# Optimization experiments

Hardware: AMD Instinct MI355X
Metric: run time of the kernel (lower is better)

The kernel has to match this reference:

```python
import jax, jax.numpy as jnp
import numpy as np

HEAD_DIM = 64

def setup_inputs() -> dict:
    key = jax.random.key(0)
    k1, k2, k3 = jax.random.split(key, 3)
    B, L, D = 2, 2048, 1024
    x = jax.random.normal(k1, (B, L, D), dtype=jnp.float32)
    # torch nn.Linear weights are [out_features, in_features]
    w_qkv = jax.random.normal(k2, (3 * D, D), dtype=jnp.float32) * (D ** -0.5)
    w_out = jax.random.normal(k3, (D, D), dtype=jnp.float32) * (D ** -0.5)
    # causal mask: True = attend (masked_fill on logical_not)
    mask = jnp.tril(jnp.ones((L, L), dtype=bool))[None].repeat(B, axis=0)
    return {"x": x, "mask": mask, "w_qkv": w_qkv, "w_out": w_out}

def reference(x, mask, w_qkv, w_out):
    B, L, D = x.shape
    H, Hd = D // HEAD_DIM, HEAD_DIM
    scale = Hd ** -0.5
    qkv = x @ w_qkv.T                               # [B, L, 3D]
    q, k, v = jnp.split(qkv, 3, axis=-1)
    # [B, L, D] -> [B, H, L, Hd]
    def split_heads(t):
        return t.reshape(B, L, H, Hd).transpose(0, 2, 1, 3)
    q, k, v = split_heads(q), split_heads(k), split_heads(v)
    attn = jnp.einsum('bhld,bhmd->bhlm', q, k) * scale  # [B, H, L, L]
    attn = jnp.where(mask[:, None, :, :], attn, -jnp.inf)
    attn = jax.nn.softmax(attn, axis=-1)
    out = jnp.einsum('bhlm,bhmd->bhld', attn, v)        # [B, H, L, Hd]
    out = out.transpose(0, 2, 1, 3).reshape(B, L, D)
    return out @ w_out.T
```

## Files before the change

### kernel.cpp

```cpp
#include <hip/hip_runtime.h>
#include <hip/hip_bf16.h>


typedef __bf16 bf16;
typedef __bf16 bf16x8 __attribute__((ext_vector_type(8)));
typedef __bf16 bf16x4 __attribute__((ext_vector_type(4)));
typedef float  f32x4  __attribute__((ext_vector_type(4)));

#define MFMA16(a, b, c) __builtin_amdgcn_mfma_f32_16x16x32_bf16(a, b, c, 0, 0, 0)

__global__ __launch_bounds__(256) void cvt_all(
    const float* __restrict__ x, const float* __restrict__ wq,
    const float* __restrict__ wo, bf16* __restrict__ dst) {
  int i = blockIdx.x * 256 + threadIdx.x;
  const float* src;
  int off;
  if (i < 1048576) {
    src = x; off = i;
  } else if (i < 1048576 + 786432) {
    src = wq; off = i - 1048576;
  } else {
    src = wo; off = i - (1048576 + 786432);
  }
  float4 v = ((const float4*)src)[off];
  bf16x4 o;
  o[0] = (bf16)v.x; o[1] = (bf16)v.y; o[2] = (bf16)v.z; o[3] = (bf16)v.w;
  ((bf16x4*)dst)[i] = o;
}

__device__ __forceinline__ void gload_lds16(const bf16* g, bf16* l) {
  __builtin_amdgcn_global_load_lds(
      (const __attribute__((address_space(1))) void*)g,
      (__attribute__((address_space(3))) void*)l, 16, 0, 0);
}

template <int ROWS>
__device__ __forceinline__ void stage_tile(const bf16* __restrict__ src, int ld,
                                           bf16* lds, int tid) {
  const int wid = tid >> 6;
#pragma unroll
  for (int i = 0; i < ROWS / 32; ++i) {
    int c = i * 256 + tid;
    int row = c >> 3;
    int slot = (c & 7) ^ (row & 7);
    gload_lds16(src + row * ld + slot * 8, lds + i * 2048 + wid * 512);
  }
}

__device__ __forceinline__ bf16x8 read_swz(const bf16* lds, int row, int kbyte) {
  int byte = row * 128 + (kbyte ^ ((row & 7) << 4));
  return *(const bf16x8*)((const char*)lds + byte);
}

template <int MODE>
__global__ __launch_bounds__(256) void gemm_nt(
    const bf16* __restrict__ A, const bf16* __restrict__ Bt,
    bf16* __restrict__ C0, bf16* __restrict__ C1, bf16* __restrict__ C2,
    float* __restrict__ Cf,
    int M, int N, int K, int nbm) {
  __shared__ bf16 ldsA[128 * 64];
  __shared__ bf16 ldsB[128 * 64];
  const int tid = threadIdx.x;
  const int lane = tid & 63, wid = tid >> 6;
  const int wr = wid >> 1, wc = wid & 1;
  const int bm = blockIdx.x % nbm, bn = blockIdx.x / nbm;
  const int l15 = lane & 15, g = lane >> 4;

  f32x4 acc[4][4] = {};
  const bf16* Ab = A + (size_t)bm * 128 * K;
  const bf16* Bb = Bt + (size_t)bn * 128 * K;

  for (int k0 = 0; k0 < K; k0 += 64) {
    __syncthreads();
    stage_tile<128>(Ab + k0, K, ldsA, tid);
    stage_tile<128>(Bb + k0, K, ldsB, tid);
    __syncthreads();
#pragma unroll
    for (int kc = 0; kc < 2; ++kc) {
      bf16x8 af[4], bfr[4];
#pragma unroll
      for (int mi = 0; mi < 4; ++mi)
        af[mi] = read_swz(ldsA, wr * 64 + mi * 16 + l15, kc * 64 + g * 16);
#pragma unroll
      for (int ni = 0; ni < 4; ++ni)
        bfr[ni] = read_swz(ldsB, wc * 64 + ni * 16 + l15, kc * 64 + g * 16);
#pragma unroll
      for (int mi = 0; mi < 4; ++mi)
#pragma unroll
        for (int ni = 0; ni < 4; ++ni)
          acc[mi][ni] = MFMA16(af[mi], bfr[ni], acc[mi][ni]);
    }
  }

  const int mbase = bm * 128 + wr * 64, nbase = bn * 128 + wc * 64;
#pragma unroll
  for (int mi = 0; mi < 4; ++mi) {
#pragma unroll
    for (int ni = 0; ni < 4; ++ni) {
#pragma unroll
      for (int r = 0; r < 4; ++r) {
        int m = mbase + mi * 16 + g * 4 + r;
        int n = nbase + ni * 16 + l15;
        if (MODE == 0) {
          Cf[(size_t)m * N + n] = acc[mi][ni][r];
        } else {
          bf16 v = (bf16)acc[mi][ni][r];
          int part = n >> 10;
          int hh = (n >> 6) & 15, hd = n & 63;
          int bb = m >> 11, ll = m & 2047;
          size_t bhb = (size_t)(bb * 16 + hh);
          if (part == 2) {
            C2[(bhb * 64 + hd) * 2048 + ll] = v;
          } else {
            bf16* dst = (part == 0) ? C0 : C1;
            dst[(bhb * 2048 + ll) * 64 + hd] = v;
          }
        }
      }
    }
  }
}

__global__ __launch_bounds__(256) void attn_fwd(
    const bf16* __restrict__ Q, const bf16* __restrict__ Kb,
    const bf16* __restrict__ Vt, bf16* __restrict__ O2) {
  __shared__ bf16 ldsK[2][64 * 64];
  __shared__ bf16 ldsVt[2][64 * 64];
  __shared__ bf16 ldsP[4][16 * 72];

  const int tid = threadIdx.x, lane = tid & 63, wid = tid >> 6;
  const int l15 = lane & 15, g = lane >> 4;
  const int qt = 31 - (blockIdx.x >> 5);
  const int bh = blockIdx.x & 31;
  const int b = bh >> 4, h = bh & 15;
  const bf16* Qh  = Q  + (size_t)bh * 2048 * 64;
  const bf16* Kh  = Kb + (size_t)bh * 2048 * 64;
  const bf16* VtH = Vt + (size_t)bh * 64 * 2048;
  const int q0 = qt * 64;
  const int qrow = q0 + wid * 16 + l15;

  bf16x8 qf[2];
#pragma unroll
  for (int dk = 0; dk < 2; ++dk)
    qf[dk] = *(const bf16x8*)(Qh + (size_t)qrow * 64 + dk * 32 + g * 8);

  float m_run = -__builtin_inff(), l_run = 0.f;
  f32x4 oacc[4] = {};

  auto step = [&](bool masked, int curb) {
    f32x4 s[4] = {};
#pragma unroll
    for (int sub = 0; sub < 4; ++sub) {
#pragma unroll
      for (int dk = 0; dk < 2; ++dk) {
        bf16x8 kf = read_swz(&ldsK[curb][0], sub * 16 + l15, dk * 64 + g * 16);
        s[sub] = MFMA16(kf, qf[dk], s[sub]);
      }
    }
    float pvv[16];
    float mtile = -__builtin_inff();
#pragma unroll
    for (int sub = 0; sub < 4; ++sub)
#pragma unroll
      for (int r = 0; r < 4; ++r) {
        float v = s[sub][r] * 0.125f;
        if (masked) {
          int kvl = sub * 16 + g * 4 + r;
          if (kvl > wid * 16 + l15) v = -__builtin_inff();
        }
        pvv[sub * 4 + r] = v;
        mtile = fmaxf(mtile, v);
      }
    mtile = fmaxf(mtile, __shfl_xor(mtile, 16));
    mtile = fmaxf(mtile, __shfl_xor(mtile, 32));
    float mnew = fmaxf(m_run, mtile);
    float alpha = __expf(m_run - mnew);
    float lsum = 0.f;
#pragma unroll
    for (int sub = 0; sub < 4; ++sub) {
      bf16x4 pb;
#pragma unroll
      for (int r = 0; r < 4; ++r) {
        float e = __expf(pvv[sub * 4 + r] - mnew);
        lsum += e;
        pb[r] = (bf16)e;
      }
      *(bf16x4*)(&ldsP[wid][l15 * 72 + sub * 16 + g * 4]) = pb;
    }
    lsum += __shfl_xor(lsum, 16);
    lsum += __shfl_xor(lsum, 32);
    l_run = alpha * l_run + lsum;
    m_run = mnew;
#pragma unroll
    for (int dsub = 0; dsub < 4; ++dsub) {
      oacc[dsub][0] *= alpha; oacc[dsub][1] *= alpha;
      oacc[dsub][2] *= alpha; oacc[dsub][3] *= alpha;
    }
#pragma unroll
    for (int kc = 0; kc < 2; ++kc) {
      bf16x8 pf = *(const bf16x8*)(&ldsP[wid][l15 * 72 + kc * 32 + g * 8]);
#pragma unroll
      for (int dsub = 0; dsub < 4; ++dsub) {
        bf16x8 vf = read_swz(&ldsVt[curb][0], dsub * 16 + l15, kc * 64 + g * 16);
        oacc[dsub] = MFMA16(vf, pf, oacc[dsub]);
      }
    }
  };

  stage_tile<64>(Kh, 64, &ldsK[0][0], tid);
  stage_tile<64>(VtH, 2048, &ldsVt[0][0], tid);
  __syncthreads();

  int cur = 0;
  for (int t = 0; t < qt; ++t) {
    stage_tile<64>(Kh + (size_t)(t + 1) * 64 * 64, 64, &ldsK[cur ^ 1][0], tid);
    stage_tile<64>(VtH + (t + 1) * 64, 2048, &ldsVt[cur ^ 1][0], tid);
    step(false, cur);
    __syncthreads();
    cur ^= 1;
  }
  step(true, cur);

  const float linv = 1.f / l_run;
#pragma unroll
  for (int dsub = 0; dsub < 4; ++dsub)
#pragma unroll
    for (int r = 0; r < 4; ++r) {
      int d = dsub * 16 + g * 4 + r;
      O2[((size_t)(b * 2048 + qrow)) * 1024 + h * 64 + d] =
          (bf16)(oacc[dsub][r] * linv);
    }
}

extern "C" void kernel_launch(void* const* d_in, const int* in_sizes, int n_in,
                              void* d_out, int out_size, void* d_ws, size_t ws_size,
                              hipStream_t stream) {
  const float* x     = (const float*)d_in[0];
  const float* w_qkv = (const float*)d_in[2];
  const float* w_out = (const float*)d_in[3];
  float* out = (float*)d_out;

  char* ws = (char*)d_ws;
  bf16* xb    = (bf16*)(ws);
  bf16* wqkvb = (bf16*)(ws + ((size_t)8 << 20));
  bf16* woutb = (bf16*)(ws + ((size_t)14 << 20));
  bf16* Qb    = (bf16*)(ws + ((size_t)16 << 20));
  bf16* Kbuf  = (bf16*)(ws + ((size_t)24 << 20));
  bf16* Vtb   = (bf16*)(ws + ((size_t)32 << 20));
  bf16* O2    = (bf16*)(ws + ((size_t)40 << 20));

  cvt_all<<<dim3(8192), 256, 0, stream>>>(x, w_qkv, w_out, xb);

  gemm_nt<1><<<dim3(32 * 24), 256, 0, stream>>>(xb, wqkvb, Qb, Kbuf, Vtb,
                                                nullptr, 4096, 3072, 1024, 32);
  attn_fwd<<<dim3(32 * 32), 256, 0, stream>>>(Qb, Kbuf, Vtb, O2);
  gemm_nt<0><<<dim3(32 * 8), 256, 0, stream>>>(O2, woutb, nullptr, nullptr,
                                               nullptr, out, 4096, 1024, 1024, 32);
}
```

Baseline: 205.7 us.

## Streamline attention softmax: exp2 with folded scale, lazy rescale, deferred row-sum reduction

Reworks the online softmax in the attention kernel. The 1/sqrt(d) scale and log2(e) are folded into one constant so exponentials use exp2f on raw scores. The accumulator rescale is skipped when no lane's running max grows, and the row-sum cross-lane reduction moves out of the loop to the end. The P staging buffer switches from padded rows to the same XOR swizzle used for K/V tiles. Together these cut per-tile ALU and shuffle work, at the cost of a wave-wide vote branch and a changed LDS addressing pattern.

Measured after the change: 199.1 us. 3.2% less time.

```diff
diff --git a/kernel.cpp b/kernel.cpp
--- a/kernel.cpp
+++ b/kernel.cpp
@@ -126,7 +126,7 @@
     const bf16* __restrict__ Vt, bf16* __restrict__ O2) {
   __shared__ bf16 ldsK[2][64 * 64];
   __shared__ bf16 ldsVt[2][64 * 64];
-  __shared__ bf16 ldsP[4][16 * 72];
+  __shared__ bf16 ldsP[4][16 * 64];
 
   const int tid = threadIdx.x, lane = tid & 63, wid = tid >> 6;
   const int l15 = lane & 15, g = lane >> 4;
@@ -139,12 +139,15 @@
   const int q0 = qt * 64;
   const int qrow = q0 + wid * 16 + l15;
 
+  const float CE = 0.18033688011112042f;
+
   bf16x8 qf[2];
 #pragma unroll
   for (int dk = 0; dk < 2; ++dk)
     qf[dk] = *(const bf16x8*)(Qh + (size_t)qrow * 64 + dk * 32 + g * 8);
 
-  float m_run = -__builtin_inff(), l_run = 0.f;
+  float m_run = -__builtin_inff();
+  float l_lane = 0.f;
   f32x4 oacc[4] = {};
 
   auto step = [&](bool masked, int curb) {
@@ -157,48 +160,51 @@
         s[sub] = MFMA16(kf, qf[dk], s[sub]);
       }
     }
-    float pvv[16];
-    float mtile = -__builtin_inff();
-#pragma unroll
-    for (int sub = 0; sub < 4; ++sub)
-#pragma unroll
-      for (int r = 0; r < 4; ++r) {
-        float v = s[sub][r] * 0.125f;
-        if (masked) {
+    if (masked) {
+#pragma unroll
+      for (int sub = 0; sub < 4; ++sub)
+#pragma unroll
+        for (int r = 0; r < 4; ++r) {
           int kvl = sub * 16 + g * 4 + r;
-          if (kvl > wid * 16 + l15) v = -__builtin_inff();
+          if (kvl > wid * 16 + l15) s[sub][r] = -__builtin_inff();
         }
-        pvv[sub * 4 + r] = v;
-        mtile = fmaxf(mtile, v);
-      }
-    mtile = fmaxf(mtile, __shfl_xor(mtile, 16));
-    mtile = fmaxf(mtile, __shfl_xor(mtile, 32));
-    float mnew = fmaxf(m_run, mtile);
-    float alpha = __expf(m_run - mnew);
+    }
+    float m0 = fmaxf(fmaxf(s[0][0], s[0][1]), fmaxf(s[0][2], s[0][3]));
+    float m1 = fmaxf(fmaxf(s[1][0], s[1][1]), fmaxf(s[1][2], s[1][3]));
+    float m2 = fmaxf(fmaxf(s[2][0], s[2][1]), fmaxf(s[2][2], s[2][3]));
+    float m3 = fmaxf(fmaxf(s[3][0], s[3][1]), fmaxf(s[3][2], s[3][3]));
+    float mt = fmaxf(fmaxf(m0, m1), fmaxf(m2, m3));
+    mt = fmaxf(mt, __shfl_xor(mt, 16));
+    mt = fmaxf(mt, __shfl_xor(mt, 32));
+    if (!__all(mt <= m_run)) {
+      float mnew = fmaxf(m_run, mt);
+      float alpha = exp2f((m_run - mnew) * CE);
+#pragma unroll
+      for (int dsub = 0; dsub < 4; ++dsub) {
+        oacc[dsub][0] *= alpha; oacc[dsub][1] *= alpha;
+        oacc[dsub][2] *= alpha; oacc[dsub][3] *= alpha;
+      }
+      l_lane *= alpha;
+      m_run = mnew;
+    }
     float lsum = 0.f;
 #pragma unroll
     for (int sub = 0; sub < 4; ++sub) {
       bf16x4 pb;
 #pragma unroll
       for (int r = 0; r < 4; ++r) {
-        float e = __expf(pvv[sub * 4 + r] - mnew);
+        float e = exp2f((s[sub][r] - m_run) * CE);
         lsum += e;
         pb[r] = (bf16)e;
       }
-      *(bf16x4*)(&ldsP[wid][l15 * 72 + sub * 16 + g * 4]) = pb;
-    }
-    lsum += __shfl_xor(lsum, 16);
-    lsum += __shfl_xor(lsum, 32);
-    l_run = alpha * l_run + lsum;
-    m_run = mnew;
-#pragma unroll
-    for (int dsub = 0; dsub < 4; ++dsub) {
-      oacc[dsub][0] *= alpha; oacc[dsub][1] *= alpha;
-      oacc[dsub][2] *= alpha; oacc[dsub][3] *= alpha;
-    }
+      int kbyte = sub * 32 + g * 8;
+      *(bf16x4*)((char*)&ldsP[wid][0] +
+                 (l15 * 128 + (kbyte ^ ((l15 & 7) << 4)))) = pb;
+    }
+    l_lane += lsum;
 #pragma unroll
     for (int kc = 0; kc < 2; ++kc) {
-      bf16x8 pf = *(const bf16x8*)(&ldsP[wid][l15 * 72 + kc * 32 + g * 8]);
+      bf16x8 pf = read_swz(&ldsP[wid][0], l15, kc * 64 + g * 16);
 #pragma unroll
       for (int dsub = 0; dsub < 4; ++dsub) {
         bf16x8 vf = read_swz(&ldsVt[curb][0], dsub * 16 + l15, kc * 64 + g * 16);
@@ -221,6 +227,9 @@
   }
   step(true, cur);
 
+  float l_run = l_lane;
+  l_run += __shfl_xor(l_run, 16);
+  l_run += __shfl_xor(l_run, 32);
   const float linv = 1.f / l_run;
 #pragma unroll
   for (int dsub = 0; dsub < 4; ++dsub)
```
